# Kernel tuning notes

Measured on AMD Instinct MI355X. Metric: run time of the kernel, lower is better.

The kernel has to match this reference:

```python
import jax, jax.numpy as jnp
import numpy as np

K_VAL = 250       # k_val
STEP_SIZE = 0.1   # step_size
TEMP = 1.0        # proposal_temp


def setup_inputs() -> dict:
    key = jax.random.key(0)
    k1, k2, k3, k4 = jax.random.split(key, 4)
    B, S, E, V = 4, 512, 64, 50257
    return {
        "gx": jax.random.normal(k1, (B, S, E), dtype=jnp.float32),
        "cur_bias": jax.random.normal(k2, (B, S, E), dtype=jnp.float32),
        "embed_weight": jax.random.normal(k3, (V, E), dtype=jnp.float32),
        "logits": jax.random.normal(k4, (B, S, V), dtype=jnp.float32),
    }


def _unfiltered_dist(gx, cur_bias, W, step_size):
    # embed-space proposal distribution (proposal_rep_space == 'embed')
    t1_1 = jnp.einsum("bse,ve->bsv", gx, W)                      # [B,S,V]
    t1_2 = jnp.einsum("bse,bse->bs", gx, cur_bias)[..., None]    # [B,S,1]
    t2_1 = jnp.sum(W * W, axis=-1)[None, None, :]                # [1,1,V]
    t2_2 = jnp.einsum("bse,ve->bsv", cur_bias, W)                # [B,S,V]
    t2_3 = jnp.sum(cur_bias * cur_bias, axis=-1)[..., None]      # [B,S,1]
    dist = 0.5 * (t1_1 - t1_2) + (t2_1 - 2.0 * t2_2 + t2_3) / step_size
    return -dist


def reference(gx, cur_bias, embed_weight, logits):
    # proposal logits over the full vocab
    unfiltered = _unfiltered_dist(gx, cur_bias, embed_weight, STEP_SIZE)  # [B,S,V]
    # candidate selection: top-k token ids by LM logits
    _, topk_ids = jax.lax.top_k(logits, K_VAL)                            # [B,S,K]
    # gather proposal logits at the candidate ids, temperature scale
    filtered = jnp.take_along_axis(unfiltered, topk_ids, axis=-1) / TEMP  # [B,S,K]
    return filtered, topk_ids
```

## Files before the change

### kernel.cpp

```cpp
#include <hip/hip_runtime.h>
#include <stdint.h>

#define BB 4
#define SS 512
#define EE 64
#define VV 50257
#define KK 250
#define NROWS (BB * SS)
#define CAP 1024
#define NB 1024

#define THRF 2.4f

typedef float float4n __attribute__((ext_vector_type(4)));
typedef unsigned long long u64;

__device__ __forceinline__ unsigned fkey(float f) {
    unsigned u = __float_as_uint(f);
    return (u & 0x80000000u) ? ~u : (u | 0x80000000u);
}

__device__ __forceinline__ unsigned binOf(unsigned key) {
    unsigned b = (key - 0xC0000000u) >> 14;
    return b > (NB - 1u) ? (NB - 1u) : b;
}

__global__ __launch_bounds__(256, 8)
void stream_kernel(const float* __restrict__ lg,
                   u64* __restrict__ cand,
                   unsigned* __restrict__ cnt)
{
    __shared__ u64 lbuf[CAP];
    __shared__ unsigned lcnt;

    const int row = blockIdx.x;
    const int tid = threadIdx.x;
    const float* rp = lg + (size_t)row * VV;

    if (tid == 0) lcnt = 0u;
    __syncthreads();

    const unsigned p  = (4u - ((unsigned)((size_t)row * VV) & 3u)) & 3u;
    const unsigned F  = (VV - p) >> 2;
    const unsigned tail0 = p + 4u * F;
    const float4n* rp4 = (const float4n*)(rp + p);

    auto emit = [&](float f, unsigned col) {
        if (f >= THRF) {
            unsigned q = atomicAdd(&lcnt, 1u);
            if (q < CAP) lbuf[q] = ((u64)fkey(f) << 32) | (unsigned)(~col);
        }
    };

    if (tid < (int)p) emit(rp[tid], tid);
    unsigned i = tid;
    for (; i + 768u < F; i += 1024u) {
        float4n a = __builtin_nontemporal_load(&rp4[i]);
        float4n b = __builtin_nontemporal_load(&rp4[i + 256u]);
        float4n c = __builtin_nontemporal_load(&rp4[i + 512u]);
        float4n d = __builtin_nontemporal_load(&rp4[i + 768u]);
        float t0 = fmaxf(fmaxf(a.x, a.y), a.z);
        float t1 = fmaxf(fmaxf(a.w, b.x), b.y);
        float t2 = fmaxf(fmaxf(b.z, b.w), c.x);
        float t3 = fmaxf(fmaxf(c.y, c.z), c.w);
        float t4 = fmaxf(fmaxf(d.x, d.y), d.z);
        float u0 = fmaxf(fmaxf(t0, t1), t2);
        float u1 = fmaxf(fmaxf(t3, t4), d.w);
        if (fmaxf(u0, u1) >= THRF) {
            unsigned c0 = p + 4u*i, c1 = p + 4u*(i+256u), c2 = p + 4u*(i+512u), c3 = p + 4u*(i+768u);
            emit(a.x, c0+0); emit(a.y, c0+1); emit(a.z, c0+2); emit(a.w, c0+3);
            emit(b.x, c1+0); emit(b.y, c1+1); emit(b.z, c1+2); emit(b.w, c1+3);
            emit(c.x, c2+0); emit(c.y, c2+1); emit(c.z, c2+2); emit(c.w, c2+3);
            emit(d.x, c3+0); emit(d.y, c3+1); emit(d.z, c3+2); emit(d.w, c3+3);
        }
    }
    for (; i < F; i += 256u) {
        float4n a = __builtin_nontemporal_load(&rp4[i]);
        if (fmaxf(fmaxf(a.x, a.y), fmaxf(a.z, a.w)) >= THRF) {
            unsigned c0 = p + 4u*i;
            emit(a.x, c0+0); emit(a.y, c0+1); emit(a.z, c0+2); emit(a.w, c0+3);
        }
    }
    for (unsigned t = tail0 + tid; t < VV; t += 256u) emit(rp[t], t);
    __syncthreads();

    const unsigned n = lcnt;
    const unsigned m = n > CAP ? CAP : n;
    for (unsigned j = tid; j < m; j += 256u)
        cand[(size_t)row * CAP + j] = lbuf[j];
    if (tid == 0) cnt[row] = n;
}

__global__ __launch_bounds__(256)
void finish_kernel(const float* __restrict__ gx,
                   const float* __restrict__ cb,
                   const float* __restrict__ W,
                   const float* __restrict__ lg,
                   const u64* __restrict__ cand,
                   const unsigned* __restrict__ cnt,
                   float* __restrict__ out0,
                   float* __restrict__ out1)
{
    __shared__ u64 sorted[CAP];
    __shared__ unsigned hist[NB];
    __shared__ unsigned offs[NB];
    __shared__ unsigned top_ids[256];
    __shared__ float u_s[EE];
    __shared__ float sCrow;
    __shared__ unsigned wtot[4];
    __shared__ unsigned lcnt, sTbin;

    const int row = blockIdx.x;
    const int tid = threadIdx.x;
    const float* rp = lg + (size_t)row * VV;

    if (tid < 64) {
        float a = gx[(size_t)row * EE + tid];
        float b = cb[(size_t)row * EE + tid];
        u_s[tid] = 0.5f * a - 20.0f * b;
        float p1 = a * b, p2 = b * b;
        #pragma unroll
        for (int d = 32; d > 0; d >>= 1) {
            p1 += __shfl_xor(p1, d, 64);
            p2 += __shfl_xor(p2, d, 64);
        }
        if (tid == 0) sCrow = 0.5f * p1 - 10.0f * p2;
    }
    for (int j = tid; j < NB; j += 256) hist[j] = 0u;
    if (tid == 0) lcnt = 0u;
    __syncthreads();

    const unsigned n = cnt[row];

    if (n >= KK && n <= CAP) {
        u64 myk[4]; unsigned myb[4];
        #pragma unroll
        for (int s = 0; s < 4; ++s) {
            unsigned j = (unsigned)tid + 256u * s;
            myk[s] = 0ull; myb[s] = 0u;
            if (j < n) {
                u64 c = cand[(size_t)row * CAP + j];
                myk[s] = c;
                unsigned b = binOf((unsigned)(c >> 32)); myb[s] = b;
                atomicAdd(&hist[b], 1u);
            }
        }
        __syncthreads();

        unsigned h0 = hist[tid*4+0], h1 = hist[tid*4+1], h2 = hist[tid*4+2], h3 = hist[tid*4+3];
        unsigned ls3 = 0, ls2 = h3, ls1 = h3 + h2, ls0 = h3 + h2 + h1;
        unsigned tot = ls0 + h0;
        const unsigned lane = (unsigned)tid & 63u, wv = (unsigned)tid >> 6;
        unsigned incl = tot;
        #pragma unroll
        for (unsigned d = 1; d < 64; d <<= 1) {
            unsigned v = __shfl_down(incl, d, 64);
            if (lane + d < 64u) incl += v;
        }
        if (lane == 0) wtot[wv] = incl;
        __syncthreads();
        unsigned above = 0;
        #pragma unroll
        for (int ww = 0; ww < 4; ++ww) if (ww > (int)wv) above += wtot[ww];
        const unsigned exclSuf = (incl - tot) + above;
        offs[tid*4+0] = exclSuf + ls0;
        offs[tid*4+1] = exclSuf + ls1;
        offs[tid*4+2] = exclSuf + ls2;
        offs[tid*4+3] = exclSuf + ls3;
        __syncthreads();

        #pragma unroll
        for (int s = 0; s < 4; ++s) {
            unsigned j = (unsigned)tid + 256u * s;
            if (j < n) {
                unsigned pos = atomicAdd(&offs[myb[s]], 1u);
                sorted[pos] = myk[s];
            }
        }
        __syncthreads();

        #pragma unroll
        for (int s = 0; s < 4; ++s) {
            unsigned j = (unsigned)tid + 256u * s;
            if (j < n) {
                unsigned b = myb[s], cntb = hist[b], base = offs[b] - cntb;
                u64 k = myk[s];
                unsigned r = base;
                for (unsigned t2 = base; t2 < base + cntb; ++t2)
                    r += (sorted[t2] > k) ? 1u : 0u;
                if (r < KK) {
                    unsigned v = ~((unsigned)k);
                    top_ids[r] = v;
                    out1[(size_t)row * KK + r] = (float)v;
                }
            }
        }
        __syncthreads();
    } else {
        const unsigned p  = (4u - ((unsigned)((size_t)row * VV) & 3u)) & 3u;
        const unsigned F  = (VV - p) >> 2;
        const unsigned tail0 = p + 4u * F;
        const float4n* rp4 = (const float4n*)(rp + p);
        unsigned* csum = offs;
        u64* lbuf = sorted;

        if (tid < (int)p) atomicAdd(&hist[fkey(rp[tid]) >> 22], 1u);
        for (unsigned j = tid; j < F; j += 256u) {
            float4n v = rp4[j];
            atomicAdd(&hist[fkey(v.x) >> 22], 1u); atomicAdd(&hist[fkey(v.y) >> 22], 1u);
            atomicAdd(&hist[fkey(v.z) >> 22], 1u); atomicAdd(&hist[fkey(v.w) >> 22], 1u);
        }
        for (unsigned t = tail0 + tid; t < VV; t += 256u) atomicAdd(&hist[fkey(rp[t]) >> 22], 1u);
        __syncthreads();

        csum[tid] = hist[tid*4] + hist[tid*4+1] + hist[tid*4+2] + hist[tid*4+3];
        __syncthreads();
        {
            unsigned g = 0;
            for (int u2 = tid + 1; u2 < 256; ++u2) g += csum[u2];
            unsigned cs = csum[tid];
            if (g < KK && g + cs >= KK) {
                unsigned cum = g;
                #pragma unroll
                for (int b2 = 3; b2 >= 0; --b2) {
                    unsigned c2 = hist[tid*4 + b2];
                    if (cum + c2 >= KK) { sTbin = (unsigned)(tid*4 + b2); break; }
                    cum += c2;
                }
            }
        }
        __syncthreads();
        const unsigned keyT = sTbin << 22;
        __syncthreads();

        auto emit2 = [&](float f, unsigned col) {
            unsigned k = fkey(f);
            if (k >= keyT) {
                unsigned q = atomicAdd(&lcnt, 1u);
                if (q < CAP) lbuf[q] = ((u64)k << 32) | (unsigned)(~col);
            }
        };
        if (tid < (int)p) emit2(rp[tid], tid);
        for (unsigned j = tid; j < F; j += 256u) {
            float4n v = rp4[j];
            unsigned ia = p + 4u*j;
            emit2(v.x, ia+0); emit2(v.y, ia+1); emit2(v.z, ia+2); emit2(v.w, ia+3);
        }
        for (unsigned t = tail0 + tid; t < VV; t += 256u) emit2(rp[t], t);
        __syncthreads();
        unsigned nf = lcnt; if (nf > CAP) nf = CAP;
        const unsigned P4 = (nf + 3u) & ~3u;
        for (unsigned j = nf + tid; j < P4; j += 256u) lbuf[j] = 0ull;
        __syncthreads();

        u64 k0 = ((unsigned)tid < nf)        ? lbuf[tid]        : 0ull;
        u64 k1 = ((unsigned)tid + 256u < nf) ? lbuf[tid + 256u] : 0ull;
        u64 k2 = ((unsigned)tid + 512u < nf) ? lbuf[tid + 512u] : 0ull;
        u64 k3 = ((unsigned)tid + 768u < nf) ? lbuf[tid + 768u] : 0ull;
        unsigned r0 = 0, r1 = 0, r2 = 0, r3 = 0;
        for (unsigned j = 0; j < P4; j += 4) {
            u64 a = lbuf[j], b = lbuf[j+1], c = lbuf[j+2], d = lbuf[j+3];
            r0 += (a > k0) + (b > k0) + (c > k0) + (d > k0);
            r1 += (a > k1) + (b > k1) + (c > k1) + (d > k1);
            r2 += (a > k2) + (b > k2) + (c > k2) + (d > k2);
            r3 += (a > k3) + (b > k3) + (c > k3) + (d > k3);
        }
        auto rec = [&](u64 k, unsigned r, bool act) {
            if (act && r < KK) {
                unsigned v = ~((unsigned)k);
                top_ids[r] = v;
                out1[(size_t)row * KK + r] = (float)v;
            }
        };
        rec(k0, r0, (unsigned)tid < nf);
        rec(k1, r1, (unsigned)tid + 256u < nf);
        rec(k2, r2, (unsigned)tid + 512u < nf);
        rec(k3, r3, (unsigned)tid + 768u < nf);
        __syncthreads();
    }

    const int grp = tid >> 4;
    const int l16 = tid & 15;
    const float4 u4 = *(const float4*)(u_s + 4 * l16);

    for (int k = grp; k < KK; k += 16) {
        unsigned v = top_ids[k];
        float4 w = *(const float4*)(W + (size_t)v * EE + 4 * l16);
        float acc = u4.x * w.x + u4.y * w.y + u4.z * w.z + u4.w * w.w
                  + 10.0f * (w.x * w.x + w.y * w.y + w.z * w.z + w.w * w.w);
        #pragma unroll
        for (int d = 8; d >= 1; d >>= 1) acc += __shfl_xor(acc, d, 16);
        if (l16 == 0) out0[(size_t)row * KK + k] = sCrow - acc;
    }
}

extern "C" void kernel_launch(void* const* d_in, const int* in_sizes, int n_in,
                              void* d_out, int out_size, void* d_ws, size_t ws_size,
                              hipStream_t stream) {
    const float* gx = (const float*)d_in[0];
    const float* cb = (const float*)d_in[1];
    const float* W  = (const float*)d_in[2];
    const float* lg = (const float*)d_in[3];
    float* out0 = (float*)d_out;
    float* out1 = out0 + (size_t)BB * SS * KK;

    unsigned* cnt = (unsigned*)d_ws;
    u64* cand = (u64*)((char*)d_ws + 32768);

    hipLaunchKernelGGL(stream_kernel, dim3(NROWS), dim3(256), 0, stream,
                       lg, cand, cnt);
    hipLaunchKernelGGL(finish_kernel, dim3(NROWS), dim3(256), 0, stream,
                       gx, cb, W, lg, cand, cnt, out0, out1);
}
```

Baseline: 98.74 us.

## Fuse candidate streaming and top-k finish into one per-row kernel

Merges the streaming threshold-filter kernel and the finish kernel into a single kernel. Candidates stay in shared memory instead of going through a global workspace, which removes the global round-trip, one launch, and the inter-kernel dependency. In exchange the fused kernel uses more shared memory per block (histograms, offsets and buffers all live at once). The launch bound of 8 blocks per CU may then not hold, lowering occupancy during the bandwidth-bound streaming phase. The fallback path re-zeroes the histogram before reusing it.

```diff
diff --git a/kernel.cpp b/kernel.cpp
--- a/kernel.cpp
+++ b/kernel.cpp
@@ -26,17 +26,39 @@
 }
 
 __global__ __launch_bounds__(256, 8)
-void stream_kernel(const float* __restrict__ lg,
-                   u64* __restrict__ cand,
-                   unsigned* __restrict__ cnt)
+void langevin_all(const float* __restrict__ gx,
+                  const float* __restrict__ cb,
+                  const float* __restrict__ W,
+                  const float* __restrict__ lg,
+                  float* __restrict__ out0,
+                  float* __restrict__ out1)
 {
     __shared__ u64 lbuf[CAP];
-    __shared__ unsigned lcnt;
+    __shared__ unsigned hist[NB];
+    __shared__ unsigned offs[NB];
+    __shared__ unsigned top_ids[256];
+    __shared__ float u_s[EE];
+    __shared__ float sCrow;
+    __shared__ unsigned wtot[4];
+    __shared__ unsigned lcnt, sTbin;
 
     const int row = blockIdx.x;
     const int tid = threadIdx.x;
     const float* rp = lg + (size_t)row * VV;
 
+    if (tid < 64) {
+        float a = gx[(size_t)row * EE + tid];
+        float b = cb[(size_t)row * EE + tid];
+        u_s[tid] = 0.5f * a - 20.0f * b;
+        float p1 = a * b, p2 = b * b;
+        #pragma unroll
+        for (int d = 32; d > 0; d >>= 1) {
+            p1 += __shfl_xor(p1, d, 64);
+            p2 += __shfl_xor(p2, d, 64);
+        }
+        if (tid == 0) sCrow = 0.5f * p1 - 10.0f * p2;
+    }
+    for (int j = tid; j < NB; j += 256) hist[j] = 0u;
     if (tid == 0) lcnt = 0u;
     __syncthreads();
 
@@ -84,53 +106,7 @@
     for (unsigned t = tail0 + tid; t < VV; t += 256u) emit(rp[t], t);
     __syncthreads();
 
-    const unsigned n = lcnt;
-    const unsigned m = n > CAP ? CAP : n;
-    for (unsigned j = tid; j < m; j += 256u)
-        cand[(size_t)row * CAP + j] = lbuf[j];
-    if (tid == 0) cnt[row] = n;
-}
-
-__global__ __launch_bounds__(256)
-void finish_kernel(const float* __restrict__ gx,
-                   const float* __restrict__ cb,
-                   const float* __restrict__ W,
-                   const float* __restrict__ lg,
-                   const u64* __restrict__ cand,
-                   const unsigned* __restrict__ cnt,
-                   float* __restrict__ out0,
-                   float* __restrict__ out1)
-{
-    __shared__ u64 sorted[CAP];
-    __shared__ unsigned hist[NB];
-    __shared__ unsigned offs[NB];
-    __shared__ unsigned top_ids[256];
-    __shared__ float u_s[EE];
-    __shared__ float sCrow;
-    __shared__ unsigned wtot[4];
-    __shared__ unsigned lcnt, sTbin;
-
-    const int row = blockIdx.x;
-    const int tid = threadIdx.x;
-    const float* rp = lg + (size_t)row * VV;
-
-    if (tid < 64) {
-        float a = gx[(size_t)row * EE + tid];
-        float b = cb[(size_t)row * EE + tid];
-        u_s[tid] = 0.5f * a - 20.0f * b;
-        float p1 = a * b, p2 = b * b;
-        #pragma unroll
-        for (int d = 32; d > 0; d >>= 1) {
-            p1 += __shfl_xor(p1, d, 64);
-            p2 += __shfl_xor(p2, d, 64);
-        }
-        if (tid == 0) sCrow = 0.5f * p1 - 10.0f * p2;
-    }
-    for (int j = tid; j < NB; j += 256) hist[j] = 0u;
-    if (tid == 0) lcnt = 0u;
-    __syncthreads();
-
-    const unsigned n = cnt[row];
+    unsigned n = lcnt;
 
     if (n >= KK && n <= CAP) {
         u64 myk[4]; unsigned myb[4];
@@ -139,8 +115,7 @@
             unsigned j = (unsigned)tid + 256u * s;
             myk[s] = 0ull; myb[s] = 0u;
             if (j < n) {
-                u64 c = cand[(size_t)row * CAP + j];
-                myk[s] = c;
+                u64 c = lbuf[j]; myk[s] = c;
                 unsigned b = binOf((unsigned)(c >> 32)); myb[s] = b;
                 atomicAdd(&hist[b], 1u);
             }
@@ -169,6 +144,7 @@
         offs[tid*4+3] = exclSuf + ls3;
         __syncthreads();
 
+        u64* sorted = lbuf;
         #pragma unroll
         for (int s = 0; s < 4; ++s) {
             unsigned j = (unsigned)tid + 256u * s;
@@ -197,12 +173,10 @@
         }
         __syncthreads();
     } else {
-        const unsigned p  = (4u - ((unsigned)((size_t)row * VV) & 3u)) & 3u;
-        const unsigned F  = (VV - p) >> 2;
-        const unsigned tail0 = p + 4u * F;
-        const float4n* rp4 = (const float4n*)(rp + p);
         unsigned* csum = offs;
-        u64* lbuf = sorted;
+        for (int j = tid; j < NB; j += 256) hist[j] = 0u;
+        if (tid == 0) lcnt = 0u;
+        __syncthreads();
 
         if (tid < (int)p) atomicAdd(&hist[fkey(rp[tid]) >> 22], 1u);
         for (unsigned j = tid; j < F; j += 256u) {
@@ -304,11 +278,6 @@
     float* out0 = (float*)d_out;
     float* out1 = out0 + (size_t)BB * SS * KK;
 
-    unsigned* cnt = (unsigned*)d_ws;
-    u64* cand = (u64*)((char*)d_ws + 32768);
-
-    hipLaunchKernelGGL(stream_kernel, dim3(NROWS), dim3(256), 0, stream,
-                       lg, cand, cnt);
-    hipLaunchKernelGGL(finish_kernel, dim3(NROWS), dim3(256), 0, stream,
-                       gx, cb, W, lg, cand, cnt, out0, out1);
-}
+    hipLaunchKernelGGL(langevin_all, dim3(NROWS), dim3(256), 0, stream,
+                       gx, cb, W, lg, out0, out1);
+}
```

Result: faster. 90.74 us (-8.1%).
